# Performance work log

Hardware: AMD Instinct MI355X
Metric: run time of the kernel (lower is better)

The kernel has to match this reference:

```python
import jax, jax.numpy as jnp
import numpy as np

TEMPORAL_WIDTH = 4  # hardcoded in GRUBlock


def causal_conv1d(x, w, b):
    """Depthwise causal temporal conv. x:[B,T,R], w:[4,R], b:[R].
    out[t] = sum_i w[i] * x[t - 3 + i] + b (zero left padding)."""
    T = x.shape[1]
    xp = jnp.pad(x, ((0, 0), (TEMPORAL_WIDTH - 1, 0), (0, 0)))
    y = b
    for i in range(TEMPORAL_WIDTH):  # tiny fixed loop over 4 taps
        y = y + w[i] * xp[:, i:i + T]
    return y


def linear_scan(a, b):
    """h_t = a_t * h_{t-1} + b_t with h_{-1}=0, via associative scan over time."""
    def comb(e1, e2):
        a1, b1 = e1
        a2, b2 = e2
        return a2 * a1, a2 * b1 + b2
    _, h = jax.lax.associative_scan(comb, (a, b), axis=1)
    return h


def setup_inputs() -> dict:
    key = jax.random.key(0)
    k1, k2, k3, k4 = jax.random.split(key, 4)
    B, T, H, R = 4, 8192, 1024, 1024
    x = jax.random.normal(k1, (B, T, H), dtype=jnp.float32)
    # lecun init: N(0, 1/sqrt(d_in)); torch Linear weight is [out, in]
    w_zh = jax.random.normal(k2, (2 * R, H), dtype=jnp.float32) / np.sqrt(H)
    w_out = jax.random.normal(k3, (H, R), dtype=jnp.float32) / np.sqrt(R)
    conv_w = jax.random.normal(k4, (TEMPORAL_WIDTH, R), dtype=jnp.float32) / np.sqrt(TEMPORAL_WIDTH)
    conv_b = jnp.zeros((R,), dtype=jnp.float32)
    return {"x": x, "w_zh": w_zh, "w_out": w_out, "conv_w": conv_w, "conv_b": conv_b}


def reference(x, w_zh, w_out, conv_w, conv_b):
    # residual causal conv
    x = x + causal_conv1d(x, conv_w, conv_b)
    # fused z/h projection: [B,T,H] @ [H,2R]
    zh = jnp.einsum('bth,rh->btr', x, w_zh)
    z, h = jnp.split(zh, 2, axis=-1)
    z = jax.nn.sigmoid(z)
    # GRU-style linear recurrence: h_t = (1-z_t) h_{t-1} + z_t h~_t
    h_o = linear_scan(1.0 - z, z * h)
    return jnp.einsum('btr,hr->bth', h_o, w_out)
```

## Files before the change

kernel.cpp:

```cpp
#include <hip/hip_runtime.h>

typedef __bf16 bf16x8 __attribute__((ext_vector_type(8)));
typedef __bf16 bf16x4 __attribute__((ext_vector_type(4)));
typedef float  f32x4  __attribute__((ext_vector_type(4)));

static constexpr int Bb = 4, T = 8192, H = 1024, R = 1024;
static constexpr int BT = Bb * T;
static constexpr int N1 = 2 * R;
static constexpr int CH = 128;
static constexpr int L  = T / CH;

__device__ __forceinline__ void g2lds16(const void* g, void* l) {
  __builtin_amdgcn_global_load_lds(
      (const __attribute__((address_space(1))) unsigned int*)g,
      (__attribute__((address_space(3))) unsigned int*)l, 16, 0, 0);
}

__global__ __launch_bounds__(256) void cast_f32_bf16(const float* __restrict__ in,
                                                     __bf16* __restrict__ out, int n4) {
  int i = blockIdx.x * 256 + threadIdx.x;
  if (i >= n4) return;
  const f32x4 v = *(const f32x4*)(in + (size_t)i * 4);
  bf16x4 o;
  o[0] = (__bf16)v[0]; o[1] = (__bf16)v[1]; o[2] = (__bf16)v[2]; o[3] = (__bf16)v[3];
  *(bf16x4*)(out + (size_t)i * 4) = o;
}

__global__ __launch_bounds__(256) void conv_residual_cast(const float* __restrict__ x,
                                                          const float* __restrict__ cw,
                                                          const float* __restrict__ cb,
                                                          __bf16* __restrict__ xc) {
  const size_t i4 = (size_t)blockIdx.x * 256 + threadIdx.x;
  const size_t v  = i4 * 4;
  const int    h  = (int)(v & (size_t)(H - 1));
  const size_t bt = v >> 10;
  const int    t  = (int)(bt & (size_t)(T - 1));
  f32x4 acc = *(const f32x4*)(cb + h);
  const f32x4 xv = *(const f32x4*)(x + v);
#pragma unroll
  for (int i = 0; i < 4; ++i) {
    const int tt = t - 3 + i;
    if (tt >= 0) {
      const f32x4 xi = *(const f32x4*)(x + (bt - 3 + i) * H + h);
      const f32x4 wi = *(const f32x4*)(cw + i * H + h);
      acc += wi * xi;
    }
  }
  acc += xv;
  bf16x4 o;
  o[0] = (__bf16)acc[0]; o[1] = (__bf16)acc[1]; o[2] = (__bf16)acc[2]; o[3] = (__bf16)acc[3];
  *(bf16x4*)(xc + v) = o;
}


#define STG_A(buf, k0, ro) g2lds16(aBase + (size_t)(r + (ro)) * K + (k0), \
                                   &sA[buf][(w8 + (ro)) * 64])
#define STG_B(buf, k0, ro) g2lds16(bBase + (size_t)(rB + (ro)) * K + (k0), \
                                   &sB[buf][(w8B + (ro)) * 64])
#define STAGE_A02(buf, kt) do { const int k0_ = (kt) * 64; STG_A(buf, k0_, 0);  STG_A(buf, k0_, 128); } while (0)
#define STAGE_A13(buf, kt) do { const int k0_ = (kt) * 64; STG_A(buf, k0_, 64); STG_A(buf, k0_, 192); } while (0)
#define STAGE_BEV(buf, kt) do { const int k0_ = (kt) * 64; STG_B(buf, k0_, 0);  STG_B(buf, k0_, 128); } while (0)
#define STAGE_BOD(buf, kt) do { const int k0_ = (kt) * 64; STG_B(buf, k0_, 32); STG_B(buf, k0_, 160); } while (0)

#define RD_A(dst, MQ, SRC) do {                                                      \
    _Pragma("unroll") for (int i_ = 0; i_ < 4; ++i_) {                               \
      const int rt_ = aRowBase + (MQ) * 64 + i_ * 16;                                \
      _Pragma("unroll") for (int ks_ = 0; ks_ < 2; ++ks_)                            \
        dst[i_][ks_] = *(const bf16x8*)&(SRC)[rt_ * 64 + (((ks_ * 4 + kg) ^ (rt_ & 7)) * 8)]; \
    } } while (0)

#define RD_B(dst, NQ, SRC) do {                                                      \
    _Pragma("unroll") for (int j_ = 0; j_ < 2; ++j_) {                               \
      const int rt_ = bRowBase + (NQ) * 32 + j_ * 16;                                \
      _Pragma("unroll") for (int ks_ = 0; ks_ < 2; ++ks_)                            \
        dst[j_][ks_] = *(const bf16x8*)&(SRC)[rt_ * 64 + (((ks_ * 4 + kg) ^ (rt_ & 7)) * 8)]; \
    } } while (0)

#define MFMA_CL(AF, BF, MQ, NQ) do {                                                 \
    __builtin_amdgcn_s_setprio(1);                                                   \
    _Pragma("unroll") for (int i_ = 0; i_ < 4; ++i_)                                 \
      _Pragma("unroll") for (int j_ = 0; j_ < 2; ++j_)                               \
        _Pragma("unroll") for (int ks_ = 0; ks_ < 2; ++ks_)                          \
          acc[(MQ) * 4 + i_][(NQ) * 2 + j_] = __builtin_amdgcn_mfma_f32_16x16x32_bf16( \
              AF[i_][ks_], BF[j_][ks_], acc[(MQ) * 4 + i_][(NQ) * 2 + j_], 0, 0, 0); \
    __builtin_amdgcn_s_setprio(0);                                                   \
  } while (0)

#define SB0 __builtin_amdgcn_sched_barrier(0)
#define BARRIER asm volatile("s_barrier" ::: "memory")
#define VMCNT4 asm volatile("s_waitcnt vmcnt(4)" ::: "memory")

template <typename OUT_T>
__global__ __launch_bounds__(512, 2) void gemm256(const __bf16* __restrict__ A,
                                                  const __bf16* __restrict__ Bm,
                                                  OUT_T* __restrict__ C,
                                                  int M, int N, int K, int nbx) {
  __shared__ __align__(16) __bf16 sA[2][256 * 64];
  __shared__ __align__(16) __bf16 sB[2][256 * 64];
  const int tid  = threadIdx.x;
  const int wave = tid >> 6;
  const int lane = tid & 63;
  const int wm = wave >> 2;
  const int wn = wave & 3;

  const int nwg = gridDim.x;
  int wg = blockIdx.x;
  wg = (wg & 7) * (nwg >> 3) + (wg >> 3);
  const int bm0 = (wg / nbx) * 256;
  const int bn0 = (wg % nbx) * 256;

  const int NT = K >> 6;

  const int r   = tid >> 3;
  const int sgc = (tid & 7) ^ (r & 7);
  const int rB  = r + (r & 32);
  const int w8  = wave * 8;
  const int w8B = w8 + (w8 & 32);
  const __bf16* aBase = A  + (size_t)bm0 * K + sgc * 8;
  const __bf16* bBase = Bm + (size_t)bn0 * K + sgc * 8;

  const int l15 = lane & 15;
  const int kg  = lane >> 4;
  const int aRowBase = wm * 128 + l15;
  const int bRowBase = wn * 64 + l15;

  f32x4 acc[8][4] = {};
  bf16x8 afA[4][2], afB[4][2], bfE[2][2], bfO[2][2];

  STAGE_BEV(0, 0);
  STAGE_A02(0, 0);
  STAGE_A13(0, 0);
  STAGE_BOD(0, 0);
  {
    const int k1 = NT > 1 ? 1 : 0;
    STAGE_BEV(1, k1);
    STAGE_A02(1, k1);
  }
  VMCNT4;
  BARRIER;
  RD_A(afA, 0, sA[0]);
  RD_B(bfE, 0, sB[0]);

  for (int kt = 0; kt < NT; ++kt) {
    const int cur = kt & 1, nxt = cur ^ 1;
    const int kt1 = (kt + 1 < NT) ? kt + 1 : NT - 1;
    const int kt2 = (kt + 2 < NT) ? kt + 2 : NT - 1;
    const __bf16* sAc = sA[cur];
    const __bf16* sBc = sB[cur];
    const __bf16* sAn = sA[nxt];
    const __bf16* sBn = sB[nxt];

    RD_B(bfO, 1, sBc);
    STAGE_A13(nxt, kt1);
    SB0;
    MFMA_CL(afA, bfE, 0, 0);
    BARRIER;
    RD_A(afB, 1, sAc);
    STAGE_BOD(nxt, kt1);
    SB0;
    MFMA_CL(afA, bfO, 0, 1);
    VMCNT4;
    BARRIER;
    RD_A(afA, 0, sAn);
    STAGE_BEV(cur, kt2);
    SB0;
    MFMA_CL(afB, bfO, 1, 1);
    BARRIER;
    STAGE_A02(cur, kt2);
    SB0;
    MFMA_CL(afB, bfE, 1, 0);
    SB0;
    RD_B(bfE, 0, sBn);
    VMCNT4;
    BARRIER;
  }

  const int orow0 = bm0 + wm * 128 + kg * 4;
  const int ocol0 = bn0 + wn * 64 + l15;
#pragma unroll
  for (int mi = 0; mi < 8; ++mi)
#pragma unroll
    for (int nj = 0; nj < 4; ++nj) {
      const size_t rbase = (size_t)(orow0 + mi * 16);
#pragma unroll
      for (int rr = 0; rr < 4; ++rr)
        C[(rbase + rr) * N + (ocol0 + nj * 16)] = (OUT_T)acc[mi][nj][rr];
    }
}

__global__ __launch_bounds__(256) void scan_pass1(const __bf16* __restrict__ zh,
                                                  float* __restrict__ aggA,
                                                  float* __restrict__ aggB) {
  const int r = (blockIdx.x * 256 + threadIdx.x) * 4;
  const int c = blockIdx.y;
  const int b = blockIdx.z;
  size_t base = ((size_t)b * T + (size_t)c * L) * N1 + r;
  float Aacc[4] = {1.f, 1.f, 1.f, 1.f};
  float Bacc[4] = {0.f, 0.f, 0.f, 0.f};
#pragma unroll 4
  for (int t = 0; t < L; ++t) {
    const bf16x4 s4 = *(const bf16x4*)(zh + base);
    const bf16x4 h4 = *(const bf16x4*)(zh + base + R);
    base += N1;
#pragma unroll
    for (int j = 0; j < 4; ++j) {
      const float z = 1.f / (1.f + __expf(-(float)s4[j]));
      const float a = 1.f - z;
      Bacc[j] = a * Bacc[j] + z * (float)h4[j];
      Aacc[j] *= a;
    }
  }
  const size_t o = ((size_t)b * CH + c) * R + r;
  *(f32x4*)(aggA + o) = f32x4{Aacc[0], Aacc[1], Aacc[2], Aacc[3]};
  *(f32x4*)(aggB + o) = f32x4{Bacc[0], Bacc[1], Bacc[2], Bacc[3]};
}

__global__ __launch_bounds__(256) void scan_pass2(const float* __restrict__ aggA,
                                                  const float* __restrict__ aggB,
                                                  float* __restrict__ carry) {
  const int idx = blockIdx.x * 256 + threadIdx.x;
  const int b = idx >> 10;
  const int r = idx & (R - 1);
  float h = 0.f;
#pragma unroll 8
  for (int c = 0; c < CH; ++c) {
    const size_t o = ((size_t)b * CH + c) * R + r;
    carry[o] = h;
    h = aggA[o] * h + aggB[o];
  }
}

__global__ __launch_bounds__(256) void scan_pass3(const __bf16* __restrict__ zh,
                                                  const float* __restrict__ carry,
                                                  __bf16* __restrict__ ho) {
  const int r = (blockIdx.x * 256 + threadIdx.x) * 4;
  const int c = blockIdx.y;
  const int b = blockIdx.z;
  size_t base  = ((size_t)b * T + (size_t)c * L) * N1 + r;
  size_t obase = ((size_t)b * T + (size_t)c * L) * R + r;
  float h[4];
  const f32x4 cv = *(const f32x4*)(carry + ((size_t)b * CH + c) * R + r);
  h[0] = cv[0]; h[1] = cv[1]; h[2] = cv[2]; h[3] = cv[3];
#pragma unroll 4
  for (int t = 0; t < L; ++t) {
    const bf16x4 s4 = *(const bf16x4*)(zh + base);
    const bf16x4 h4 = *(const bf16x4*)(zh + base + R);
    base += N1;
    bf16x4 o;
#pragma unroll
    for (int j = 0; j < 4; ++j) {
      const float z = 1.f / (1.f + __expf(-(float)s4[j]));
      h[j] = (1.f - z) * h[j] + z * (float)h4[j];
      o[j] = (__bf16)h[j];
    }
    *(bf16x4*)(ho + obase) = o;
    obase += R;
  }
}

extern "C" void kernel_launch(void* const* d_in, const int* in_sizes, int n_in,
                              void* d_out, int out_size, void* d_ws, size_t ws_size,
                              hipStream_t stream) {
  const float* x      = (const float*)d_in[0];
  const float* w_zh   = (const float*)d_in[1];
  const float* w_out  = (const float*)d_in[2];
  const float* conv_w = (const float*)d_in[3];
  const float* conv_b = (const float*)d_in[4];
  float* out = (float*)d_out;

  char* ws = (char*)d_ws;
  size_t off = 0;
  __bf16* wzh_b  = (__bf16*)(ws + off); off += (size_t)N1 * H * 2;
  __bf16* wout_b = (__bf16*)(ws + off); off += (size_t)H * R * 2;
  __bf16* xc     = (__bf16*)(ws + off); off += (size_t)BT * H * 2;
  __bf16* zh     = (__bf16*)(ws + off); off += (size_t)BT * N1 * 2;
  float*  carry  = (float*)(ws + off);  off += (size_t)Bb * CH * R * 4;
  float*  aggA   = (float*)wzh_b;
  float*  aggB   = (float*)((char*)wzh_b + (size_t)Bb * CH * R * 4);
  __bf16* ho = xc;

  cast_f32_bf16<<<(N1 * H / 4 + 255) / 256, 256, 0, stream>>>(w_zh, wzh_b, N1 * H / 4);
  cast_f32_bf16<<<(H * R / 4 + 255) / 256, 256, 0, stream>>>(w_out, wout_b, H * R / 4);
  conv_residual_cast<<<BT * H / 4 / 256, 256, 0, stream>>>(x, conv_w, conv_b, xc);
  gemm256<__bf16><<<(BT / 256) * (N1 / 256), 512, 0, stream>>>(xc, wzh_b, zh, BT, N1, H, N1 / 256);
  scan_pass1<<<dim3(R / 4 / 256, CH, Bb), 256, 0, stream>>>(zh, aggA, aggB);
  scan_pass2<<<Bb * R / 256, 256, 0, stream>>>(aggA, aggB, carry);
  scan_pass3<<<dim3(R / 4 / 256, CH, Bb), 256, 0, stream>>>(zh, carry, ho);
  gemm256<float><<<(BT / 256) * (H / 256), 512, 0, stream>>>(ho, wout_b, out, BT, H, R, H / 256);
}
```

Before: 568.8 us.

## Switch GEMM to 32x32x16 MFMA, unroll k-loop by two, restructure conv and scan pass2

```diff
diff --git a/kernel.cpp b/kernel.cpp
--- a/kernel.cpp
+++ b/kernel.cpp
@@ -3,6 +3,7 @@
 typedef __bf16 bf16x8 __attribute__((ext_vector_type(8)));
 typedef __bf16 bf16x4 __attribute__((ext_vector_type(4)));
 typedef float  f32x4  __attribute__((ext_vector_type(4)));
+typedef float  f32x16 __attribute__((ext_vector_type(16)));
 
 static constexpr int Bb = 4, T = 8192, H = 1024, R = 1024;
 static constexpr int BT = Bb * T;
@@ -30,26 +31,33 @@
                                                           const float* __restrict__ cw,
                                                           const float* __restrict__ cb,
                                                           __bf16* __restrict__ xc) {
-  const size_t i4 = (size_t)blockIdx.x * 256 + threadIdx.x;
-  const size_t v  = i4 * 4;
-  const int    h  = (int)(v & (size_t)(H - 1));
-  const size_t bt = v >> 10;
-  const int    t  = (int)(bt & (size_t)(T - 1));
-  f32x4 acc = *(const f32x4*)(cb + h);
-  const f32x4 xv = *(const f32x4*)(x + v);
-#pragma unroll
-  for (int i = 0; i < 4; ++i) {
-    const int tt = t - 3 + i;
-    if (tt >= 0) {
-      const f32x4 xi = *(const f32x4*)(x + (bt - 3 + i) * H + h);
-      const f32x4 wi = *(const f32x4*)(cw + i * H + h);
-      acc += wi * xi;
-    }
-  }
-  acc += xv;
-  bf16x4 o;
-  o[0] = (__bf16)acc[0]; o[1] = (__bf16)acc[1]; o[2] = (__bf16)acc[2]; o[3] = (__bf16)acc[3];
-  *(bf16x4*)(xc + v) = o;
+  const int h  = threadIdx.x * 4;
+  const int b  = blockIdx.y;
+  const int t0 = blockIdx.x * 8;
+  const f32x4 w0 = *(const f32x4*)(cw + 0 * H + h);
+  const f32x4 w1 = *(const f32x4*)(cw + 1 * H + h);
+  const f32x4 w2 = *(const f32x4*)(cw + 2 * H + h);
+  const f32x4 w3 = *(const f32x4*)(cw + 3 * H + h);
+  const f32x4 bias = *(const f32x4*)(cb + h);
+  size_t base = ((size_t)b * T + t0) * H + h;
+  f32x4 xm3, xm2, xm1;
+  if (t0 >= 3) {
+    xm3 = *(const f32x4*)(x + base - 3 * H);
+    xm2 = *(const f32x4*)(x + base - 2 * H);
+    xm1 = *(const f32x4*)(x + base - 1 * H);
+  } else {
+    xm3 = f32x4{0, 0, 0, 0}; xm2 = xm3; xm1 = xm3;
+  }
+#pragma unroll
+  for (int tt = 0; tt < 8; ++tt) {
+    const f32x4 x0 = *(const f32x4*)(x + base);
+    const f32x4 acc = x0 + bias + w0 * xm3 + w1 * xm2 + w2 * xm1 + w3 * x0;
+    bf16x4 o;
+    o[0] = (__bf16)acc[0]; o[1] = (__bf16)acc[1]; o[2] = (__bf16)acc[2]; o[3] = (__bf16)acc[3];
+    *(bf16x4*)(xc + base) = o;
+    xm3 = xm2; xm2 = xm1; xm1 = x0;
+    base += H;
+  }
 }
 
 
@@ -63,32 +71,44 @@
 #define STAGE_BOD(buf, kt) do { const int k0_ = (kt) * 64; STG_B(buf, k0_, 32); STG_B(buf, k0_, 160); } while (0)
 
 #define RD_A(dst, MQ, SRC) do {                                                      \
-    _Pragma("unroll") for (int i_ = 0; i_ < 4; ++i_) {                               \
-      const int rt_ = aRowBase + (MQ) * 64 + i_ * 16;                                \
-      _Pragma("unroll") for (int ks_ = 0; ks_ < 2; ++ks_)                            \
-        dst[i_][ks_] = *(const bf16x8*)&(SRC)[rt_ * 64 + (((ks_ * 4 + kg) ^ (rt_ & 7)) * 8)]; \
+    _Pragma("unroll") for (int m_ = 0; m_ < 2; ++m_) {                               \
+      const int rt_ = aRowBase + (MQ) * 64 + m_ * 32;                                \
+      _Pragma("unroll") for (int ks_ = 0; ks_ < 4; ++ks_)                            \
+        dst[m_][ks_] = *(const bf16x8*)&(SRC)[rt_ * 64 + (((2 * ks_ + kb) ^ (rt_ & 7)) * 8)]; \
     } } while (0)
 
 #define RD_B(dst, NQ, SRC) do {                                                      \
-    _Pragma("unroll") for (int j_ = 0; j_ < 2; ++j_) {                               \
-      const int rt_ = bRowBase + (NQ) * 32 + j_ * 16;                                \
-      _Pragma("unroll") for (int ks_ = 0; ks_ < 2; ++ks_)                            \
-        dst[j_][ks_] = *(const bf16x8*)&(SRC)[rt_ * 64 + (((ks_ * 4 + kg) ^ (rt_ & 7)) * 8)]; \
-    } } while (0)
+    const int rt_ = bRowBase + (NQ) * 32;                                            \
+    _Pragma("unroll") for (int ks_ = 0; ks_ < 4; ++ks_)                              \
+      dst[ks_] = *(const bf16x8*)&(SRC)[rt_ * 64 + (((2 * ks_ + kb) ^ (rt_ & 7)) * 8)]; \
+  } while (0)
 
 #define MFMA_CL(AF, BF, MQ, NQ) do {                                                 \
     __builtin_amdgcn_s_setprio(1);                                                   \
-    _Pragma("unroll") for (int i_ = 0; i_ < 4; ++i_)                                 \
-      _Pragma("unroll") for (int j_ = 0; j_ < 2; ++j_)                               \
-        _Pragma("unroll") for (int ks_ = 0; ks_ < 2; ++ks_)                          \
-          acc[(MQ) * 4 + i_][(NQ) * 2 + j_] = __builtin_amdgcn_mfma_f32_16x16x32_bf16( \
-              AF[i_][ks_], BF[j_][ks_], acc[(MQ) * 4 + i_][(NQ) * 2 + j_], 0, 0, 0); \
+    _Pragma("unroll") for (int ks_ = 0; ks_ < 4; ++ks_)                              \
+      _Pragma("unroll") for (int m_ = 0; m_ < 2; ++m_)                               \
+        acc[(MQ) * 2 + m_][NQ] = __builtin_amdgcn_mfma_f32_32x32x16_bf16(            \
+            AF[m_][ks_], BF[ks_], acc[(MQ) * 2 + m_][NQ], 0, 0, 0);                  \
     __builtin_amdgcn_s_setprio(0);                                                   \
   } while (0)
 
 #define SB0 __builtin_amdgcn_sched_barrier(0)
 #define BARRIER asm volatile("s_barrier" ::: "memory")
 #define VMCNT4 asm volatile("s_waitcnt vmcnt(4)" ::: "memory")
+
+#define TILE_BODY(KT, CI, NI) do {                                                   \
+    const int kt1 = ((KT) + 1 < NT) ? (KT) + 1 : NT - 1;                             \
+    const int kt2 = ((KT) + 2 < NT) ? (KT) + 2 : NT - 1;                             \
+     RD_B(bfO, 1, sB[CI]); STAGE_A13(NI, kt1); SB0;                         \
+    MFMA_CL(afA, bfE, 0, 0); BARRIER;                                                \
+     RD_A(afB, 1, sA[CI]); STAGE_BOD(NI, kt1); SB0;                         \
+    MFMA_CL(afA, bfO, 0, 1); VMCNT4; BARRIER;                                        \
+     RD_A(afA, 0, sA[NI]); STAGE_BEV(CI, kt2); SB0;                         \
+    MFMA_CL(afB, bfO, 1, 1); BARRIER;                                                \
+     STAGE_A02(CI, kt2); SB0;                                               \
+    MFMA_CL(afB, bfE, 1, 0); SB0;                                                    \
+    RD_B(bfE, 0, sB[NI]); VMCNT4; BARRIER;                                           \
+  } while (0)
 
 template <typename OUT_T>
 __global__ __launch_bounds__(512, 2) void gemm256(const __bf16* __restrict__ A,
@@ -119,13 +139,13 @@
   const __bf16* aBase = A  + (size_t)bm0 * K + sgc * 8;
   const __bf16* bBase = Bm + (size_t)bn0 * K + sgc * 8;
 
-  const int l15 = lane & 15;
-  const int kg  = lane >> 4;
-  const int aRowBase = wm * 128 + l15;
-  const int bRowBase = wn * 64 + l15;
-
-  f32x4 acc[8][4] = {};
-  bf16x8 afA[4][2], afB[4][2], bfE[2][2], bfO[2][2];
+  const int ln = lane & 31;
+  const int kb = lane >> 5;
+  const int aRowBase = wm * 128 + ln;
+  const int bRowBase = wn * 64 + ln;
+
+  f32x16 acc[4][2] = {};
+  bf16x8 afA[2][4], afB[2][4], bfE[4], bfO[4];
 
   STAGE_BEV(0, 0);
   STAGE_A02(0, 0);
@@ -141,50 +161,23 @@
   RD_A(afA, 0, sA[0]);
   RD_B(bfE, 0, sB[0]);
 
-  for (int kt = 0; kt < NT; ++kt) {
-    const int cur = kt & 1, nxt = cur ^ 1;
-    const int kt1 = (kt + 1 < NT) ? kt + 1 : NT - 1;
-    const int kt2 = (kt + 2 < NT) ? kt + 2 : NT - 1;
-    const __bf16* sAc = sA[cur];
-    const __bf16* sBc = sB[cur];
-    const __bf16* sAn = sA[nxt];
-    const __bf16* sBn = sB[nxt];
-
-    RD_B(bfO, 1, sBc);
-    STAGE_A13(nxt, kt1);
-    SB0;
-    MFMA_CL(afA, bfE, 0, 0);
-    BARRIER;
-    RD_A(afB, 1, sAc);
-    STAGE_BOD(nxt, kt1);
-    SB0;
-    MFMA_CL(afA, bfO, 0, 1);
-    VMCNT4;
-    BARRIER;
-    RD_A(afA, 0, sAn);
-    STAGE_BEV(cur, kt2);
-    SB0;
-    MFMA_CL(afB, bfO, 1, 1);
-    BARRIER;
-    STAGE_A02(cur, kt2);
-    SB0;
-    MFMA_CL(afB, bfE, 1, 0);
-    SB0;
-    RD_B(bfE, 0, sBn);
-    VMCNT4;
-    BARRIER;
-  }
-
-  const int orow0 = bm0 + wm * 128 + kg * 4;
-  const int ocol0 = bn0 + wn * 64 + l15;
-#pragma unroll
-  for (int mi = 0; mi < 8; ++mi)
-#pragma unroll
-    for (int nj = 0; nj < 4; ++nj) {
-      const size_t rbase = (size_t)(orow0 + mi * 16);
-#pragma unroll
-      for (int rr = 0; rr < 4; ++rr)
-        C[(rbase + rr) * N + (ocol0 + nj * 16)] = (OUT_T)acc[mi][nj][rr];
+  for (int kt = 0; kt < NT; kt += 2) {
+    TILE_BODY(kt, 0, 1);
+    TILE_BODY(kt + 1, 1, 0);
+  }
+
+  const int orow0 = bm0 + wm * 128;
+  const int ocol0 = bn0 + wn * 64;
+#pragma unroll
+  for (int a = 0; a < 4; ++a)
+#pragma unroll
+    for (int j = 0; j < 2; ++j) {
+      const int col = ocol0 + j * 32 + ln;
+#pragma unroll
+      for (int rr = 0; rr < 16; ++rr) {
+        const int row = orow0 + a * 32 + (rr & 3) + 8 * (rr >> 2) + 4 * kb;
+        C[(size_t)row * N + col] = (OUT_T)acc[a][j][rr];
+      }
     }
 }
 
@@ -215,10 +208,10 @@
   *(f32x4*)(aggB + o) = f32x4{Bacc[0], Bacc[1], Bacc[2], Bacc[3]};
 }
 
-__global__ __launch_bounds__(256) void scan_pass2(const float* __restrict__ aggA,
-                                                  const float* __restrict__ aggB,
-                                                  float* __restrict__ carry) {
-  const int idx = blockIdx.x * 256 + threadIdx.x;
+__global__ __launch_bounds__(64) void scan_pass2(const float* __restrict__ aggA,
+                                                 const float* __restrict__ aggB,
+                                                 float* __restrict__ carry) {
+  const int idx = blockIdx.x * 64 + threadIdx.x;
   const int b = idx >> 10;
   const int r = idx & (R - 1);
   float h = 0.f;
@@ -281,10 +274,10 @@
 
   cast_f32_bf16<<<(N1 * H / 4 + 255) / 256, 256, 0, stream>>>(w_zh, wzh_b, N1 * H / 4);
   cast_f32_bf16<<<(H * R / 4 + 255) / 256, 256, 0, stream>>>(w_out, wout_b, H * R / 4);
-  conv_residual_cast<<<BT * H / 4 / 256, 256, 0, stream>>>(x, conv_w, conv_b, xc);
+  conv_residual_cast<<<dim3(T / 8, Bb), 256, 0, stream>>>(x, conv_w, conv_b, xc);
   gemm256<__bf16><<<(BT / 256) * (N1 / 256), 512, 0, stream>>>(xc, wzh_b, zh, BT, N1, H, N1 / 256);
   scan_pass1<<<dim3(R / 4 / 256, CH, Bb), 256, 0, stream>>>(zh, aggA, aggB);
-  scan_pass2<<<Bb * R / 256, 256, 0, stream>>>(aggA, aggB, carry);
+  scan_pass2<<<Bb * R / 64, 64, 0, stream>>>(aggA, aggB, carry);
   scan_pass3<<<dim3(R / 4 / 256, CH, Bb), 256, 0, stream>>>(zh, carry, ho);
   gemm256<float><<<(BT / 256) * (H / 256), 512, 0, stream>>>(ho, wout_b, out, BT, H, R, H / 256);
 }
```

Result: faster. 552.7 us (-2.8%).
